# Kernel tuning notes

Hardware: AMD Instinct MI355X
Metric: run time of the kernel (lower is better)

The kernel has to match this reference:

```python
import jax, jax.numpy as jnp
import numpy as np

NEG = -1000000.0

def setup_inputs() -> dict:
    key = jax.random.key(0)
    k1, k2, k3, k4, k5 = jax.random.split(key, 5)
    B, Lq, Lm, Din, Dout = 8, 2048, 2048, 1024, 1024
    query = jax.random.normal(k1, (B, Lq, Din), dtype=jnp.float32)
    memories = jax.random.normal(k2, (B, Lm, Dout), dtype=jnp.float32)
    mask = jax.random.randint(k3, (B, Lq, Lm), 0, 2, dtype=jnp.int32)
    # Linear(in_features=1024, out_features=1024)
    bound = 1.0 / np.sqrt(Din)
    W = jax.random.uniform(k4, (Dout, Din), minval=-bound, maxval=bound, dtype=jnp.float32)
    b = jax.random.uniform(k5, (Dout,), minval=-bound, maxval=bound, dtype=jnp.float32)
    return {"query": query, "memories": memories, "mask": mask, "W": W, "b": b}

def reference(query, memories, mask, W, b):
    # projected query: [B, Lq, Dout]
    q = jnp.einsum('bqi,oi->bqo', query, W) + b
    # additive binary mask: 1 -> 0, 0 -> -1e6
    add_mask = (1.0 - mask.astype(q.dtype)) * NEG
    # unscaled Luong scores: [B, Lq, Lm]
    logits = jnp.einsum('bqd,bmd->bqm', q, memories) + add_mask
    weights = jax.nn.softmax(logits, axis=-1)
    out = jnp.einsum('bqm,bmd->bqd', weights, memories)
    return out
```

## Files before the change

### kernel.cpp

```cpp
#include <hip/hip_runtime.h>

typedef float    f32x4 __attribute__((ext_vector_type(4)));
typedef _Float16 f16x4 __attribute__((ext_vector_type(4)));
typedef _Float16 f16x8 __attribute__((ext_vector_type(8)));

__device__ __forceinline__ void gload16(const _Float16* g, _Float16* l) {
  __builtin_amdgcn_global_load_lds(
      (__attribute__((address_space(1))) void*)g,
      (__attribute__((address_space(3))) void*)l, 16, 0, 0);
}

template <typename TOUT, bool BIAS>
__global__ __launch_bounds__(256) void gemm128h(
    const _Float16* __restrict__ A, const _Float16* __restrict__ B,
    const float* __restrict__ bias, TOUT* __restrict__ Cp,
    int M, int N, int K, long sA, long sB, long sC) {
  __shared__ _Float16 As[128 * 32];
  __shared__ _Float16 Bs[128 * 32];
  const int tid = threadIdx.x;
  const int lane = tid & 63, wv = tid >> 6;
  const int wr = (wv >> 1) * 64, wc = (wv & 1) * 64;
  const int l15 = lane & 15, k8 = (lane >> 4) * 8;
  const int m0 = blockIdx.y * 128, n0 = blockIdx.x * 128;
  const _Float16* Ab = A + (size_t)blockIdx.z * sA;
  const _Float16* Bb = B + (size_t)blockIdx.z * sB;

  const int srow = lane >> 2;
  const int sc8  = (lane & 3) * 8;

  f32x4 acc[4][4] = {};

  for (int k0 = 0; k0 < K; k0 += 32) {
    #pragma unroll
    for (int r = 0; r < 2; r++) {
      const int t = wv * 2 + r;
      const int row = t * 16 + srow;
      gload16(&Ab[(size_t)(m0 + row) * K + k0 + sc8], &As[t * 512]);
      gload16(&Bb[(size_t)(n0 + row) * K + k0 + sc8], &Bs[t * 512]);
    }
    __syncthreads();
    f16x8 af[4], bf[4];
    #pragma unroll
    for (int i = 0; i < 4; i++)
      af[i] = *(const f16x8*)&As[(wr + i * 16 + l15) * 32 + k8];
    #pragma unroll
    for (int j = 0; j < 4; j++)
      bf[j] = *(const f16x8*)&Bs[(wc + j * 16 + l15) * 32 + k8];
    #pragma unroll
    for (int i = 0; i < 4; i++)
      #pragma unroll
      for (int j = 0; j < 4; j++)
        acc[i][j] = __builtin_amdgcn_mfma_f32_16x16x32_f16(af[i], bf[j],
                                                           acc[i][j], 0, 0, 0);
    __syncthreads();
  }

  TOUT* C = Cp + (size_t)blockIdx.z * sC;
  const int q4 = (lane >> 4) * 4;
  #pragma unroll
  for (int j = 0; j < 4; j++) {
    int col = n0 + wc + j * 16 + l15;
    float bb = BIAS ? bias[col] : 0.0f;
    #pragma unroll
    for (int i = 0; i < 4; i++) {
      int rowb = m0 + wr + i * 16 + q4;
      #pragma unroll
      for (int rr = 0; rr < 4; rr++)
        C[(size_t)(rowb + rr) * N + col] = (TOUT)(acc[i][j][rr] + bb);
    }
  }
}

__global__ __launch_bounds__(256) void transpose16_kernel(
    const _Float16* __restrict__ src, _Float16* __restrict__ dst) {
  const int Lm = 2048, D = 1024;
  __shared__ _Float16 tile[64 * 64];
  const int d0 = blockIdx.x * 64, m0 = blockIdx.y * 64;
  const _Float16* s = src + (size_t)blockIdx.z * Lm * D;
  _Float16*       d = dst + (size_t)blockIdx.z * D * Lm;
  const int tid = threadIdx.x;
  #pragma unroll
  for (int it = 0; it < 2; it++) {
    int idx = tid + it * 256;
    int mm = idx >> 3, g = idx & 7;
    int pg = g ^ ((mm >> 3) & 7);
    *(f16x8*)&tile[mm * 64 + pg * 8] =
        *(const f16x8*)&s[(size_t)(m0 + mm) * D + d0 + g * 8];
  }
  __syncthreads();
  #pragma unroll
  for (int it = 0; it < 2; it++) {
    int idx = tid + it * 256;
    int dd = idx >> 3, mc = (idx & 7) * 8;
    f16x8 h;
    #pragma unroll
    for (int j = 0; j < 8; j++) {
      int row = mc + j;
      int pg = (dd >> 3) ^ ((row >> 3) & 7);
      h[j] = tile[row * 64 + pg * 8 + (dd & 7)];
    }
    *(f16x8*)&d[(size_t)(d0 + dd) * Lm + m0 + mc] = h;
  }
}

__global__ __launch_bounds__(256) void softmax_kernel(
    const int* __restrict__ mask, _Float16* __restrict__ wbuf) {
  const int Lm = 2048;
  size_t row = blockIdx.x;
  _Float16* wr = wbuf + row * Lm;
  const int* mr = mask + row * Lm;
  int tid = threadIdx.x;
  f16x8 lv = *(const f16x8*)&wr[tid * 8];
  int4 ma = *(const int4*)&mr[tid * 8];
  int4 mb = *(const int4*)&mr[tid * 8 + 4];
  int mk[8] = {ma.x, ma.y, ma.z, ma.w, mb.x, mb.y, mb.z, mb.w};
  float v[8];
  float mx = -3.0e38f;
  #pragma unroll
  for (int i = 0; i < 8; i++) {
    float l = (float)lv[i];
    if (mk[i] == 0) l += -1000000.0f;
    v[i] = l;
    mx = fmaxf(mx, l);
  }
  #pragma unroll
  for (int off = 32; off > 0; off >>= 1) mx = fmaxf(mx, __shfl_down(mx, off, 64));
  __shared__ float red[4];
  int wv = tid >> 6;
  if ((tid & 63) == 0) red[wv] = mx;
  __syncthreads();
  mx = fmaxf(fmaxf(red[0], red[1]), fmaxf(red[2], red[3]));
  __syncthreads();
  float s = 0.f;
  #pragma unroll
  for (int i = 0; i < 8; i++) { v[i] = __expf(v[i] - mx); s += v[i]; }
  #pragma unroll
  for (int off = 32; off > 0; off >>= 1) s += __shfl_down(s, off, 64);
  if ((tid & 63) == 0) red[wv] = s;
  __syncthreads();
  float inv = 1.0f / (red[0] + red[1] + red[2] + red[3]);
  f16x8 o;
  #pragma unroll
  for (int i = 0; i < 8; i++) o[i] = (_Float16)(v[i] * inv);
  *(f16x8*)&wr[tid * 8] = o;
}

__global__ __launch_bounds__(256) void cvt8_kernel(const float* __restrict__ x,
                                                   _Float16* __restrict__ y) {
  size_t i = (size_t)(blockIdx.x * 256 + threadIdx.x) * 8;
  f32x4 a = *(const f32x4*)&x[i];
  f32x4 b = *(const f32x4*)&x[i + 4];
  f16x8 h = {(_Float16)a[0], (_Float16)a[1], (_Float16)a[2], (_Float16)a[3],
             (_Float16)b[0], (_Float16)b[1], (_Float16)b[2], (_Float16)b[3]};
  *(f16x8*)&y[i] = h;
}

extern "C" void kernel_launch(void* const* d_in, const int* in_sizes, int n_in,
                              void* d_out, int out_size, void* d_ws, size_t ws_size,
                              hipStream_t stream) {
  const float* query = (const float*)d_in[0];
  const float* mem   = (const float*)d_in[1];
  const int*   mask  = (const int*)d_in[2];
  const float* W     = (const float*)d_in[3];
  const float* bias  = (const float*)d_in[4];
  float* out = (float*)d_out;

  char* ws = (char*)d_ws;
  _Float16* qproj  = (_Float16*)ws;
  _Float16* memT   = (_Float16*)ws;
  _Float16* queryh = (_Float16*)(ws + (size_t)32 * 1024 * 1024);
  _Float16* Wh     = (_Float16*)(ws + (size_t)64 * 1024 * 1024);
  _Float16* wbuf   = (_Float16*)(ws + (size_t)32 * 1024 * 1024);
  _Float16* memh   = (_Float16*)d_out;

  const long LQK = 2048L * 1024, LQM = 2048L * 2048;

  cvt8_kernel<<<dim3(512),  256, 0, stream>>>(W, Wh);
  cvt8_kernel<<<dim3(8192), 256, 0, stream>>>(query, queryh);
  cvt8_kernel<<<dim3(8192), 256, 0, stream>>>(mem, memh);
  gemm128h<_Float16, true><<<dim3(8, 128, 1), 256, 0, stream>>>(
      queryh, Wh, bias, qproj, 16384, 1024, 1024, 0, 0, 0);
  gemm128h<_Float16, false><<<dim3(16, 16, 8), 256, 0, stream>>>(
      qproj, memh, nullptr, wbuf, 2048, 2048, 1024, LQK, LQK, LQM);
  softmax_kernel<<<dim3(16384), 256, 0, stream>>>(mask, wbuf);
  transpose16_kernel<<<dim3(16, 32, 8), 256, 0, stream>>>(memh, memT);
  gemm128h<float, false><<<dim3(8, 16, 8), 256, 0, stream>>>(
      wbuf, memT, nullptr, out, 2048, 1024, 2048, LQM, LQK, LQK);
}
```

Baseline: 592.0 us.

## Replace 128-tile GEMM with double-buffered 256x256 tile GEMM using swizzled LDS

Replaces the simple 128x128, K=32 GEMM, which synchronized on every step, with a 256x256-tile, 512-thread kernel. The new kernel double-buffers K=64 stages in 128KB of LDS and prefetches the next tile while MFMAs run, using s_setprio and explicit vmcnt waits. An XOR swizzle on LDS addresses avoids bank conflicts. The aim is more data reuse per block and hiding global load latency, at the cost of more registers, one block per CU, and fewer blocks per GEMM.

Result: faster. 514.2 us (-13.1%).

```diff
diff --git a/kernel.cpp b/kernel.cpp
--- a/kernel.cpp
+++ b/kernel.cpp
@@ -4,69 +4,165 @@
 typedef _Float16 f16x4 __attribute__((ext_vector_type(4)));
 typedef _Float16 f16x8 __attribute__((ext_vector_type(8)));
 
-__device__ __forceinline__ void gload16(const _Float16* g, _Float16* l) {
+__device__ __forceinline__ void gload16(const void* g, void* l) {
   __builtin_amdgcn_global_load_lds(
-      (__attribute__((address_space(1))) void*)g,
+      (const __attribute__((address_space(1))) void*)g,
       (__attribute__((address_space(3))) void*)l, 16, 0, 0);
 }
 
+#define MFMA16(d, a, b) __builtin_amdgcn_mfma_f32_16x16x32_f16(a, b, d, 0, 0, 0)
+
+template <bool STG>
+__device__ __forceinline__ void ktile256(
+    char* L, int d, size_t go,
+    const char* aSrc0, const char* aSrc1,
+    const char* bSrc0, const char* bSrc1,
+    int ldsStage, int wr, int wc, int l15, int rcb,
+    f32x4 (&acc)[8][4]) {
+  const char* Ab0 = L + d * 32768;
+  const char* Bb0 = L + 65536 + d * 32768;
+  const int dn = d ^ 1;
+  f16x8 af[8], bf[2];
+
+  #pragma unroll
+  for (int m = 0; m < 8; m++)
+    af[m] = *(const f16x8*)(Ab0 + (wr + m * 16 + l15) * 64 + rcb);
+  #pragma unroll
+  for (int n = 0; n < 2; n++)
+    bf[n] = *(const f16x8*)(Bb0 + (wc + n * 16 + l15) * 64 + rcb);
+  if constexpr (STG) {
+    char* dst = L + dn * 32768 + ldsStage;
+    gload16(aSrc0 + go, dst);
+    gload16(aSrc1 + go, dst + 1024);
+  }
+  __builtin_amdgcn_s_barrier();
+  __builtin_amdgcn_s_setprio(1);
+  #pragma unroll
+  for (int m = 0; m < 8; m++) {
+    acc[m][0] = MFMA16(acc[m][0], af[m], bf[0]);
+    acc[m][1] = MFMA16(acc[m][1], af[m], bf[1]);
+  }
+  __builtin_amdgcn_s_setprio(0);
+  __builtin_amdgcn_s_barrier();
+
+  #pragma unroll
+  for (int n = 0; n < 2; n++)
+    bf[n] = *(const f16x8*)(Bb0 + (wc + (2 + n) * 16 + l15) * 64 + rcb);
+  if constexpr (STG) {
+    char* dst = L + 65536 + dn * 32768 + ldsStage;
+    gload16(bSrc0 + go, dst);
+    gload16(bSrc1 + go, dst + 1024);
+    asm volatile("s_waitcnt vmcnt(4)" ::: "memory");
+  } else {
+    asm volatile("s_waitcnt vmcnt(0)" ::: "memory");
+  }
+  __builtin_amdgcn_s_barrier();
+  __builtin_amdgcn_s_setprio(1);
+  #pragma unroll
+  for (int m = 0; m < 8; m++) {
+    acc[m][2] = MFMA16(acc[m][2], af[m], bf[0]);
+    acc[m][3] = MFMA16(acc[m][3], af[m], bf[1]);
+  }
+  __builtin_amdgcn_s_setprio(0);
+  __builtin_amdgcn_s_barrier();
+
+  #pragma unroll
+  for (int m = 0; m < 8; m++)
+    af[m] = *(const f16x8*)(Ab0 + 16384 + (wr + m * 16 + l15) * 64 + rcb);
+  #pragma unroll
+  for (int n = 0; n < 2; n++)
+    bf[n] = *(const f16x8*)(Bb0 + 16384 + (wc + n * 16 + l15) * 64 + rcb);
+  if constexpr (STG) {
+    char* dst = L + dn * 32768 + 16384 + ldsStage;
+    gload16(aSrc0 + go + 64, dst);
+    gload16(aSrc1 + go + 64, dst + 1024);
+  }
+  __builtin_amdgcn_s_barrier();
+  __builtin_amdgcn_s_setprio(1);
+  #pragma unroll
+  for (int m = 0; m < 8; m++) {
+    acc[m][0] = MFMA16(acc[m][0], af[m], bf[0]);
+    acc[m][1] = MFMA16(acc[m][1], af[m], bf[1]);
+  }
+  __builtin_amdgcn_s_setprio(0);
+  __builtin_amdgcn_s_barrier();
+
+  #pragma unroll
+  for (int n = 0; n < 2; n++)
+    bf[n] = *(const f16x8*)(Bb0 + 16384 + (wc + (2 + n) * 16 + l15) * 64 + rcb);
+  if constexpr (STG) {
+    char* dst = L + 65536 + dn * 32768 + 16384 + ldsStage;
+    gload16(bSrc0 + go + 64, dst);
+    gload16(bSrc1 + go + 64, dst + 1024);
+    asm volatile("s_waitcnt vmcnt(4)" ::: "memory");
+  }
+  __builtin_amdgcn_s_barrier();
+  __builtin_amdgcn_s_setprio(1);
+  #pragma unroll
+  for (int m = 0; m < 8; m++) {
+    acc[m][2] = MFMA16(acc[m][2], af[m], bf[0]);
+    acc[m][3] = MFMA16(acc[m][3], af[m], bf[1]);
+  }
+  __builtin_amdgcn_s_setprio(0);
+  __builtin_amdgcn_s_barrier();
+}
+
 template <typename TOUT, bool BIAS>
-__global__ __launch_bounds__(256) void gemm128h(
+__global__ __launch_bounds__(512) void gemm256(
     const _Float16* __restrict__ A, const _Float16* __restrict__ B,
     const float* __restrict__ bias, TOUT* __restrict__ Cp,
     int M, int N, int K, long sA, long sB, long sC) {
-  __shared__ _Float16 As[128 * 32];
-  __shared__ _Float16 Bs[128 * 32];
+  __shared__ _Float16 lds[65536];
+  char* const L = (char*)lds;
   const int tid = threadIdx.x;
-  const int lane = tid & 63, wv = tid >> 6;
-  const int wr = (wv >> 1) * 64, wc = (wv & 1) * 64;
-  const int l15 = lane & 15, k8 = (lane >> 4) * 8;
-  const int m0 = blockIdx.y * 128, n0 = blockIdx.x * 128;
+  const int w = tid >> 6, l = tid & 63;
+  const int l15 = l & 15, q = l >> 4;
+  const int wr = (w >> 2) * 128, wc = (w & 3) * 64;
+  const int m0 = blockIdx.y * 256, n0 = blockIdx.x * 256;
   const _Float16* Ab = A + (size_t)blockIdx.z * sA;
   const _Float16* Bb = B + (size_t)blockIdx.z * sB;
 
-  const int srow = lane >> 2;
-  const int sc8  = (lane & 3) * 8;
-
-  f32x4 acc[4][4] = {};
-
-  for (int k0 = 0; k0 < K; k0 += 32) {
-    #pragma unroll
-    for (int r = 0; r < 2; r++) {
-      const int t = wv * 2 + r;
-      const int row = t * 16 + srow;
-      gload16(&Ab[(size_t)(m0 + row) * K + k0 + sc8], &As[t * 512]);
-      gload16(&Bb[(size_t)(n0 + row) * K + k0 + sc8], &Bs[t * 512]);
-    }
-    __syncthreads();
-    f16x8 af[4], bf[4];
-    #pragma unroll
-    for (int i = 0; i < 4; i++)
-      af[i] = *(const f16x8*)&As[(wr + i * 16 + l15) * 32 + k8];
-    #pragma unroll
-    for (int j = 0; j < 4; j++)
-      bf[j] = *(const f16x8*)&Bs[(wc + j * 16 + l15) * 32 + k8];
-    #pragma unroll
-    for (int i = 0; i < 4; i++)
-      #pragma unroll
-      for (int j = 0; j < 4; j++)
-        acc[i][j] = __builtin_amdgcn_mfma_f32_16x16x32_f16(af[i], bf[j],
-                                                           acc[i][j], 0, 0, 0);
-    __syncthreads();
-  }
+  const int scb = ((l & 3) ^ q) << 4;
+  const int sr0 = w * 32 + (l >> 2);
+  const char* aSrc0 = (const char*)(Ab + (size_t)(m0 + sr0) * K) + scb;
+  const char* aSrc1 = (const char*)(Ab + (size_t)(m0 + sr0 + 16) * K) + scb;
+  const char* bSrc0 = (const char*)(Bb + (size_t)(n0 + sr0) * K) + scb;
+  const char* bSrc1 = (const char*)(Bb + (size_t)(n0 + sr0 + 16) * K) + scb;
+  const int ldsStage = w * 2048;
+  const int rcb = ((q ^ (l15 >> 2)) << 4);
+
+  f32x4 acc[8][4] = {};
+  const int NT = K >> 6;
+
+  {
+    char* dA = L + ldsStage;
+    char* dB = L + 65536 + ldsStage;
+    gload16(aSrc0, dA);       gload16(aSrc1, dA + 1024);
+    gload16(bSrc0, dB);       gload16(bSrc1, dB + 1024);
+    gload16(aSrc0 + 64, dA + 16384); gload16(aSrc1 + 64, dA + 16384 + 1024);
+    gload16(bSrc0 + 64, dB + 16384); gload16(bSrc1 + 64, dB + 16384 + 1024);
+    asm volatile("s_waitcnt vmcnt(4)" ::: "memory");
+  }
+  __builtin_amdgcn_s_barrier();
+
+  for (int t = 0; t < NT - 1; ++t)
+    ktile256<true>(L, t & 1, (size_t)(t + 1) * 128, aSrc0, aSrc1, bSrc0, bSrc1,
+                   ldsStage, wr, wc, l15, rcb, acc);
+  ktile256<false>(L, (NT - 1) & 1, 0, aSrc0, aSrc1, bSrc0, bSrc1,
+                  ldsStage, wr, wc, l15, rcb, acc);
 
   TOUT* C = Cp + (size_t)blockIdx.z * sC;
-  const int q4 = (lane >> 4) * 4;
-  #pragma unroll
-  for (int j = 0; j < 4; j++) {
-    int col = n0 + wc + j * 16 + l15;
+  const int q4 = q * 4;
+  #pragma unroll
+  for (int n = 0; n < 4; n++) {
+    int col = n0 + wc + n * 16 + l15;
     float bb = BIAS ? bias[col] : 0.0f;
     #pragma unroll
-    for (int i = 0; i < 4; i++) {
-      int rowb = m0 + wr + i * 16 + q4;
+    for (int m = 0; m < 8; m++) {
+      int rowb = m0 + wr + m * 16 + q4;
       #pragma unroll
       for (int rr = 0; rr < 4; rr++)
-        C[(size_t)(rowb + rr) * N + col] = (TOUT)(acc[i][j][rr] + bb);
+        C[(size_t)(rowb + rr) * N + col] = (TOUT)(acc[m][n][rr] + bb);
     }
   }
 }
@@ -178,12 +274,12 @@
   cvt8_kernel<<<dim3(512),  256, 0, stream>>>(W, Wh);
   cvt8_kernel<<<dim3(8192), 256, 0, stream>>>(query, queryh);
   cvt8_kernel<<<dim3(8192), 256, 0, stream>>>(mem, memh);
-  gemm128h<_Float16, true><<<dim3(8, 128, 1), 256, 0, stream>>>(
+  gemm256<_Float16, true><<<dim3(4, 64, 1), 512, 0, stream>>>(
       queryh, Wh, bias, qproj, 16384, 1024, 1024, 0, 0, 0);
-  gemm128h<_Float16, false><<<dim3(16, 16, 8), 256, 0, stream>>>(
+  gemm256<_Float16, false><<<dim3(8, 8, 8), 512, 0, stream>>>(
       qproj, memh, nullptr, wbuf, 2048, 2048, 1024, LQK, LQK, LQM);
   softmax_kernel<<<dim3(16384), 256, 0, stream>>>(mask, wbuf);
   transpose16_kernel<<<dim3(16, 32, 8), 256, 0, stream>>>(memh, memT);
-  gemm128h<float, false><<<dim3(8, 16, 8), 256, 0, stream>>>(
+  gemm256<float, false><<<dim3(4, 8, 8), 512, 0, stream>>>(
       wbuf, memT, nullptr, out, 2048, 1024, 2048, LQM, LQK, LQK);
 }
```

## Replace GEMM with double-buffered 256x128 tile kernel, swizzled LDS and XCD remap

Applied to the files above, without the earlier changes.

Replaces the 128x128 single-buffered GEMM with a 512-thread, 256x128-tile kernel. It double-buffers LDS so the next k-slice's global-to-LDS loads overlap the current slice's MFMAs. It also XOR-swizzles the LDS layout to avoid bank conflicts, remaps workgroup IDs across XCDs for better L2 locality, and raises wave priority around the MFMA block. It uses more LDS per block (48 KB) and halves the block count, which may reduce occupancy or leave the last wave of blocks unbalanced.

After: 477.9 us. 19.3% less time.

```diff
diff --git a/kernel.cpp b/kernel.cpp
--- a/kernel.cpp
+++ b/kernel.cpp
@@ -4,69 +4,118 @@
 typedef _Float16 f16x4 __attribute__((ext_vector_type(4)));
 typedef _Float16 f16x8 __attribute__((ext_vector_type(8)));
 
-__device__ __forceinline__ void gload16(const _Float16* g, _Float16* l) {
+__device__ __forceinline__ void gload16(const void* g, void* l) {
   __builtin_amdgcn_global_load_lds(
-      (__attribute__((address_space(1))) void*)g,
+      (const __attribute__((address_space(1))) void*)g,
       (__attribute__((address_space(3))) void*)l, 16, 0, 0);
 }
 
+#define MFMA16(d, a, b) __builtin_amdgcn_mfma_f32_16x16x32_f16(a, b, d, 0, 0, 0)
+#define VMCNT0() asm volatile("s_waitcnt vmcnt(0)" ::: "memory")
+#define BAR()    __builtin_amdgcn_s_barrier()
+
 template <typename TOUT, bool BIAS>
-__global__ __launch_bounds__(256) void gemm128h(
+__global__ __launch_bounds__(512, 4) void gemm256x128(
     const _Float16* __restrict__ A, const _Float16* __restrict__ B,
     const float* __restrict__ bias, TOUT* __restrict__ Cp,
     int M, int N, int K, long sA, long sB, long sC) {
-  __shared__ _Float16 As[128 * 32];
-  __shared__ _Float16 Bs[128 * 32];
+  __shared__ _Float16 lds[24576];
+  char* const L = (char*)lds;
   const int tid = threadIdx.x;
-  const int lane = tid & 63, wv = tid >> 6;
-  const int wr = (wv >> 1) * 64, wc = (wv & 1) * 64;
-  const int l15 = lane & 15, k8 = (lane >> 4) * 8;
-  const int m0 = blockIdx.y * 128, n0 = blockIdx.x * 128;
-  const _Float16* Ab = A + (size_t)blockIdx.z * sA;
-  const _Float16* Bb = B + (size_t)blockIdx.z * sB;
-
-  const int srow = lane >> 2;
-  const int sc8  = (lane & 3) * 8;
+  const int w = tid >> 6, l = tid & 63;
+  const int l15 = l & 15, q = l >> 4;
+  const int wr = (w >> 1) * 64, wc = (w & 1) * 64;
+
+  const int gx = gridDim.x, gy = gridDim.y;
+  const int nwg = gx * gy * gridDim.z;
+  const int lin = (blockIdx.z * gy + blockIdx.y) * gx + blockIdx.x;
+  const int li = (lin & 7) * (nwg >> 3) + (lin >> 3);
+  const int bx = li % gx;
+  const int t1 = li / gx;
+  const int by = t1 % gy;
+  const int bz = t1 / gy;
+
+  const int m0 = by * 256, n0 = bx * 128;
+  const _Float16* Ab = A + (size_t)bz * sA;
+  const _Float16* Bb = B + (size_t)bz * sB;
+
+  const int scb = (((l & 3) ^ ((l >> 3) & 3)) << 4);
+  const int sr = w * 16 + (l >> 2);
+  const long rowB = (long)K * 2;
+  const char* aS  = (const char*)Ab + (size_t)(m0 + sr) * rowB + scb;
+  const char* aS2 = aS + 128 * rowB;
+  const char* bS  = (const char*)Bb + (size_t)(n0 + sr) * rowB + scb;
+  const int stW = w * 1024;
+  const int rcb = ((q ^ ((l15 >> 1) & 3)) << 4);
+  const int aOff = (wr + l15) * 64 + rcb;
+  const int bOff = 32768 + (wc + l15) * 64 + rcb;
 
   f32x4 acc[4][4] = {};
-
-  for (int k0 = 0; k0 < K; k0 += 32) {
-    #pragma unroll
-    for (int r = 0; r < 2; r++) {
-      const int t = wv * 2 + r;
-      const int row = t * 16 + srow;
-      gload16(&Ab[(size_t)(m0 + row) * K + k0 + sc8], &As[t * 512]);
-      gload16(&Bb[(size_t)(n0 + row) * K + k0 + sc8], &Bs[t * 512]);
-    }
-    __syncthreads();
+  const int NT = K >> 5;
+
+  gload16(aS, L + stW);
+  gload16(aS2, L + stW + 8192);
+  gload16(bS, L + 32768 + stW);
+  VMCNT0();
+  BAR();
+
+  for (int t = 0; t < NT - 1; ++t) {
+    const int d = t & 1, dn = d ^ 1;
+    const long go = (long)(t + 1) * 64;
+    char* sbA = L + dn * 16384 + stW;
+    char* sbB = L + 32768 + dn * 8192 + stW;
+    gload16(aS + go, sbA);
+    gload16(aS2 + go, sbA + 8192);
+    gload16(bS + go, sbB);
+
+    const char* pA = L + d * 16384 + aOff;
+    const char* pB = L + d * 8192 + bOff;
     f16x8 af[4], bf[4];
     #pragma unroll
-    for (int i = 0; i < 4; i++)
-      af[i] = *(const f16x8*)&As[(wr + i * 16 + l15) * 32 + k8];
-    #pragma unroll
-    for (int j = 0; j < 4; j++)
-      bf[j] = *(const f16x8*)&Bs[(wc + j * 16 + l15) * 32 + k8];
-    #pragma unroll
-    for (int i = 0; i < 4; i++)
+    for (int m = 0; m < 4; m++) af[m] = *(const f16x8*)(pA + m * 1024);
+    #pragma unroll
+    for (int n = 0; n < 4; n++) bf[n] = *(const f16x8*)(pB + n * 1024);
+
+    __builtin_amdgcn_s_setprio(1);
+    #pragma unroll
+    for (int m = 0; m < 4; m++)
       #pragma unroll
-      for (int j = 0; j < 4; j++)
-        acc[i][j] = __builtin_amdgcn_mfma_f32_16x16x32_f16(af[i], bf[j],
-                                                           acc[i][j], 0, 0, 0);
-    __syncthreads();
-  }
-
-  TOUT* C = Cp + (size_t)blockIdx.z * sC;
-  const int q4 = (lane >> 4) * 4;
-  #pragma unroll
-  for (int j = 0; j < 4; j++) {
-    int col = n0 + wc + j * 16 + l15;
+      for (int n = 0; n < 4; n++)
+        acc[m][n] = MFMA16(acc[m][n], af[m], bf[n]);
+    __builtin_amdgcn_s_setprio(0);
+
+    VMCNT0();
+    BAR();
+  }
+
+  {
+    const int d = (NT - 1) & 1;
+    const char* pA = L + d * 16384 + aOff;
+    const char* pB = L + d * 8192 + bOff;
+    f16x8 af[4], bf[4];
+    #pragma unroll
+    for (int m = 0; m < 4; m++) af[m] = *(const f16x8*)(pA + m * 1024);
+    #pragma unroll
+    for (int n = 0; n < 4; n++) bf[n] = *(const f16x8*)(pB + n * 1024);
+    #pragma unroll
+    for (int m = 0; m < 4; m++)
+      #pragma unroll
+      for (int n = 0; n < 4; n++)
+        acc[m][n] = MFMA16(acc[m][n], af[m], bf[n]);
+  }
+
+  TOUT* C = Cp + (size_t)bz * sC;
+  const int q4 = q * 4;
+  #pragma unroll
+  for (int n = 0; n < 4; n++) {
+    int col = n0 + wc + n * 16 + l15;
     float bb = BIAS ? bias[col] : 0.0f;
     #pragma unroll
-    for (int i = 0; i < 4; i++) {
-      int rowb = m0 + wr + i * 16 + q4;
+    for (int m = 0; m < 4; m++) {
+      int rowb = m0 + wr + m * 16 + q4;
       #pragma unroll
       for (int rr = 0; rr < 4; rr++)
-        C[(size_t)(rowb + rr) * N + col] = (TOUT)(acc[i][j][rr] + bb);
+        C[(size_t)(rowb + rr) * N + col] = (TOUT)(acc[m][n][rr] + bb);
     }
   }
 }
@@ -178,12 +227,12 @@
   cvt8_kernel<<<dim3(512),  256, 0, stream>>>(W, Wh);
   cvt8_kernel<<<dim3(8192), 256, 0, stream>>>(query, queryh);
   cvt8_kernel<<<dim3(8192), 256, 0, stream>>>(mem, memh);
-  gemm128h<_Float16, true><<<dim3(8, 128, 1), 256, 0, stream>>>(
+  gemm256x128<_Float16, true><<<dim3(8, 64, 1), 512, 0, stream>>>(
       queryh, Wh, bias, qproj, 16384, 1024, 1024, 0, 0, 0);
-  gemm128h<_Float16, false><<<dim3(16, 16, 8), 256, 0, stream>>>(
+  gemm256x128<_Float16, false><<<dim3(16, 8, 8), 512, 0, stream>>>(
       qproj, memh, nullptr, wbuf, 2048, 2048, 1024, LQK, LQK, LQM);
   softmax_kernel<<<dim3(16384), 256, 0, stream>>>(mask, wbuf);
   transpose16_kernel<<<dim3(16, 32, 8), 256, 0, stream>>>(memh, memT);
-  gemm128h<float, false><<<dim3(8, 16, 8), 256, 0, stream>>>(
+  gemm256x128<float, false><<<dim3(8, 8, 8), 512, 0, stream>>>(
       wbuf, memT, nullptr, out, 2048, 1024, 2048, LQM, LQK, LQK);
 }
```
